# Kernel optimization log

Hardware: AMD Instinct MI355X
Metric: run time of the kernel (lower is better)

The kernel has to match this reference:

```python
import jax, jax.numpy as jnp
import numpy as np

LN_EPS = 1e-5  # torch nn.LayerNorm default


def setup_inputs() -> dict:
    key = jax.random.key(0)
    kx, kw = jax.random.split(key)
    tokens, d_in, d_out = 8192, 4096, 16384
    x = jax.random.normal(kx, (tokens, d_in), dtype=jnp.float32)
    # nn.Linear weight layout: [out_features, in_features]
    W = jax.random.normal(kw, (d_out, d_in), dtype=jnp.float32) * (1.0 / np.sqrt(d_in))
    return {"x": x, "W": W}


def reference(x, W):
    # LayerNorm over last dim, no affine params (elementwise_affine=False)
    mean = jnp.mean(x, axis=-1, keepdims=True)
    var = jnp.mean(jnp.square(x - mean), axis=-1, keepdims=True)  # biased, as torch LN
    xn = (x - mean) * jax.lax.rsqrt(var + LN_EPS)
    # Linear (no bias): [tokens, d_in] @ [d_in, d_out]
    y = jnp.einsum("td,od->to", xn, W)
    return jax.nn.sigmoid(y)
```

## Files before the change

kernel.cpp:

```cpp
#include <hip/hip_runtime.h>
#include <hip/hip_bf16.h>
#include <stdint.h>

#define TOKENS 8192
#define DIN    4096
#define DOUT   16384

#define BM 256
#define BN 256
#define BKT 64
#define NT (DIN / BKT)
#define NJ (NT / 2)

typedef short s16x8 __attribute__((ext_vector_type(8)));
typedef float f32x4 __attribute__((ext_vector_type(4)));

#define AS1 __attribute__((address_space(1)))
#define AS3 __attribute__((address_space(3)))
#define VMCNT(n)  asm volatile("s_waitcnt vmcnt(" #n ")" ::: "memory")
#define LGKM0()   asm volatile("s_waitcnt lgkmcnt(0)" ::: "memory")
#define SCHEDB()  __builtin_amdgcn_sched_barrier(0)
#define BAR()     __builtin_amdgcn_s_barrier()

__device__ __forceinline__ unsigned short f2bf(float f) {
  unsigned int u = __float_as_uint(f);
  u += 0x7fffu + ((u >> 16) & 1u);
  return (unsigned short)(u >> 16);
}

__global__ __launch_bounds__(256) void ln_kernel(const float* __restrict__ x,
                                                 unsigned short* __restrict__ xn) {
  const int row = blockIdx.x;
  const float4* xr = reinterpret_cast<const float4*>(x + (size_t)row * DIN);
  float4 v[4];
  float sum = 0.f, ssq = 0.f;
#pragma unroll
  for (int i = 0; i < 4; ++i) {
    v[i] = xr[threadIdx.x + i * 256];
    sum += v[i].x + v[i].y + v[i].z + v[i].w;
    ssq += v[i].x * v[i].x + v[i].y * v[i].y + v[i].z * v[i].z + v[i].w * v[i].w;
  }
#pragma unroll
  for (int off = 32; off > 0; off >>= 1) {
    sum += __shfl_xor(sum, off, 64);
    ssq += __shfl_xor(ssq, off, 64);
  }
  __shared__ float red[8];
  const int wid = threadIdx.x >> 6;
  if ((threadIdx.x & 63) == 0) { red[wid] = sum; red[wid + 4] = ssq; }
  __syncthreads();
  sum = red[0] + red[1] + red[2] + red[3];
  ssq = red[4] + red[5] + red[6] + red[7];
  const float mean = sum * (1.f / DIN);
  const float var  = ssq * (1.f / DIN) - mean * mean;
  const float rs   = rsqrtf(var + 1e-5f);
  ushort4* xo = reinterpret_cast<ushort4*>(xn + (size_t)row * DIN);
#pragma unroll
  for (int i = 0; i < 4; ++i) {
    ushort4 o;
    o.x = f2bf((v[i].x - mean) * rs);
    o.y = f2bf((v[i].y - mean) * rs);
    o.z = f2bf((v[i].z - mean) * rs);
    o.w = f2bf((v[i].w - mean) * rs);
    xo[threadIdx.x + i * 256] = o;
  }
}

__global__ __launch_bounds__(256) void cvt_kernel(const float* __restrict__ W,
                                                  unsigned short* __restrict__ Wb) {
  const size_t i = (size_t)blockIdx.x * 256 + threadIdx.x;
  float4 v = reinterpret_cast<const float4*>(W)[i];
  ushort4 o;
  o.x = f2bf(v.x); o.y = f2bf(v.y); o.z = f2bf(v.z); o.w = f2bf(v.w);
  reinterpret_cast<ushort4*>(Wb)[i] = o;
}

__global__ __launch_bounds__(512, 2) void gemm_sig(const unsigned short* __restrict__ A,
                                                   const unsigned short* __restrict__ B,
                                                   float* __restrict__ C) {
  __shared__ unsigned short Asl[2 * 256 * 64];
  __shared__ unsigned short Bsl[2 * 256 * 64];

  const int bid = blockIdx.x;
  const int cpx = gridDim.x >> 3;
  const int swz = (bid & 7) * cpx + (bid >> 3);
  const int bm = swz & 31;
  const int bn = swz >> 5;

  const int tid  = threadIdx.x;
  const int wid  = tid >> 6;
  const int lane = tid & 63;
  const int wr = wid >> 2, wc = wid & 3;

  const unsigned short* gA = A + (size_t)bm * BM * DIN;
  const unsigned short* gB = B + (size_t)bn * BN * DIN;

  const int l8 = lane >> 3, l7 = lane & 7;
  const int csw = l7 ^ l8;
  const unsigned short* sA0 = gA + (size_t)(wid * 8 + l8) * DIN + csw * 8;
  const unsigned short* sA1 = sA0 + (size_t)64 * DIN;
  const unsigned short* sB0 = gB + (size_t)(wid * 8 + l8) * DIN + csw * 8;
  const unsigned short* sB1 = sB0 + (size_t)64 * DIN;
  const int dOfs = wid * 512;

#define STG_A(p, h, kt) do { \
  __builtin_amdgcn_global_load_lds((const AS1 void*)(sA0 + (size_t)(h) * 128 * DIN + (kt) * BKT), \
      (AS3 void*)(Asl + ((p) * 256 + (h) * 128) * 64 + dOfs), 16, 0, 0); \
  __builtin_amdgcn_global_load_lds((const AS1 void*)(sA1 + (size_t)(h) * 128 * DIN + (kt) * BKT), \
      (AS3 void*)(Asl + ((p) * 256 + (h) * 128 + 64) * 64 + dOfs), 16, 0, 0); } while (0)
#define STG_B(p, h, kt) do { \
  __builtin_amdgcn_global_load_lds((const AS1 void*)(sB0 + (size_t)(h) * 128 * DIN + (kt) * BKT), \
      (AS3 void*)(Bsl + ((p) * 256 + (h) * 128) * 64 + dOfs), 16, 0, 0); \
  __builtin_amdgcn_global_load_lds((const AS1 void*)(sB1 + (size_t)(h) * 128 * DIN + (kt) * BKT), \
      (AS3 void*)(Bsl + ((p) * 256 + (h) * 128 + 64) * 64 + dOfs), 16, 0, 0); } while (0)

  const int aBase = (wr * 128 + (lane & 15)) * 64;
  const int bBase = (wc * 64 + (lane & 15)) * 64;
  const int slt0 = (((lane >> 4)) ^ l7) * 8;
  const int slt1 = (((lane >> 4) + 4) ^ l7) * 8;

  s16x8 af[4][2], bf[4][2];
  f32x4 acc[8][4] = {};

#define LDA(p, MB) do { _Pragma("unroll") for (int mm = 0; mm < 4; ++mm) { \
    const unsigned short* _b = Asl + (p) * 16384 + aBase + ((MB) + mm) * 1024; \
    af[mm][0] = *reinterpret_cast<const s16x8*>(_b + slt0); \
    af[mm][1] = *reinterpret_cast<const s16x8*>(_b + slt1); } } while (0)
#define LDB(p, NB) do { _Pragma("unroll") for (int nn = 0; nn < 2; ++nn) { \
    const unsigned short* _b = Bsl + (p) * 16384 + bBase + ((NB) + nn) * 1024; \
    bf[(NB) + nn][0] = *reinterpret_cast<const s16x8*>(_b + slt0); \
    bf[(NB) + nn][1] = *reinterpret_cast<const s16x8*>(_b + slt1); } } while (0)

#define QUAD(MB, NB) do { _Pragma("unroll") for (int mm = 0; mm < 4; ++mm) { \
    _Pragma("unroll") for (int nn = 0; nn < 2; ++nn) { \
      acc[(MB)+mm][(NB)+nn] = __builtin_amdgcn_mfma_f32_16x16x32_bf16(af[mm][0], bf[(NB)+nn][0], acc[(MB)+mm][(NB)+nn], 0, 0, 0); \
      acc[(MB)+mm][(NB)+nn] = __builtin_amdgcn_mfma_f32_16x16x32_bf16(af[mm][1], bf[(NB)+nn][1], acc[(MB)+mm][(NB)+nn], 0, 0, 0); } } } while (0)

#define PH_TOP()  SCHEDB(); BAR()
#define PH_BOT()  LGKM0(); SCHEDB(); BAR()

  STG_B(0, 0, 0); STG_B(0, 1, 0); STG_A(0, 0, 0); STG_A(0, 1, 0);
  STG_B(1, 0, 1); STG_B(1, 1, 1);
  VMCNT(4); SCHEDB(); BAR();

  for (int j = 0; j < NJ - 1; ++j) {
    const int t1 = 2 * j + 1, t2 = 2 * j + 2, t3 = 2 * j + 3;
    LDA(0, 0); LDB(0, 0); STG_A(1, 0, t1); PH_TOP();
    __builtin_amdgcn_s_setprio(1); QUAD(0, 0); __builtin_amdgcn_s_setprio(0); PH_BOT();
    LDB(0, 2); STG_A(1, 1, t1); PH_TOP();
    __builtin_amdgcn_s_setprio(1); QUAD(0, 2); __builtin_amdgcn_s_setprio(0); PH_BOT();
    LDA(0, 4); STG_B(0, 0, t2); PH_TOP();
    __builtin_amdgcn_s_setprio(1); QUAD(4, 0); __builtin_amdgcn_s_setprio(0); PH_BOT();
    STG_B(0, 1, t2); PH_TOP();
    __builtin_amdgcn_s_setprio(1); QUAD(4, 2); __builtin_amdgcn_s_setprio(0);
    LGKM0(); VMCNT(4); SCHEDB(); BAR();
    LDA(1, 0); LDB(1, 0); STG_A(0, 0, t2); PH_TOP();
    __builtin_amdgcn_s_setprio(1); QUAD(0, 0); __builtin_amdgcn_s_setprio(0); PH_BOT();
    LDB(1, 2); STG_A(0, 1, t2); PH_TOP();
    __builtin_amdgcn_s_setprio(1); QUAD(0, 2); __builtin_amdgcn_s_setprio(0); PH_BOT();
    LDA(1, 4); STG_B(1, 0, t3); PH_TOP();
    __builtin_amdgcn_s_setprio(1); QUAD(4, 0); __builtin_amdgcn_s_setprio(0); PH_BOT();
    STG_B(1, 1, t3); PH_TOP();
    __builtin_amdgcn_s_setprio(1); QUAD(4, 2); __builtin_amdgcn_s_setprio(0);
    LGKM0(); VMCNT(4); SCHEDB(); BAR();
  }

  {
    const int t1 = NT - 1;
    LDA(0, 0); LDB(0, 0); STG_A(1, 0, t1); PH_TOP();
    __builtin_amdgcn_s_setprio(1); QUAD(0, 0); __builtin_amdgcn_s_setprio(0); PH_BOT();
    LDB(0, 2); STG_A(1, 1, t1); PH_TOP();
    __builtin_amdgcn_s_setprio(1); QUAD(0, 2); __builtin_amdgcn_s_setprio(0); PH_BOT();
    LDA(0, 4); PH_TOP();
    __builtin_amdgcn_s_setprio(1); QUAD(4, 0); __builtin_amdgcn_s_setprio(0); PH_BOT();
    PH_TOP();
    __builtin_amdgcn_s_setprio(1); QUAD(4, 2); __builtin_amdgcn_s_setprio(0);
    LGKM0(); VMCNT(0); SCHEDB(); BAR();
    LDA(1, 0); LDB(1, 0); PH_TOP();
    __builtin_amdgcn_s_setprio(1); QUAD(0, 0); __builtin_amdgcn_s_setprio(0); PH_BOT();
    LDB(1, 2); PH_TOP();
    __builtin_amdgcn_s_setprio(1); QUAD(0, 2); __builtin_amdgcn_s_setprio(0); PH_BOT();
    LDA(1, 4); PH_TOP();
    __builtin_amdgcn_s_setprio(1); QUAD(4, 0); __builtin_amdgcn_s_setprio(0); PH_BOT();
    __builtin_amdgcn_s_setprio(1); QUAD(4, 2); __builtin_amdgcn_s_setprio(0);
  }

#undef STG_A
#undef STG_B
#undef LDA
#undef LDB
#undef QUAD
#undef PH_TOP
#undef PH_BOT

  const int crow0 = bm * BM + wr * 128 + (lane >> 4) * 4;
  const int ccol0 = bn * BN + wc * 64 + (lane & 15);
#pragma unroll
  for (int m = 0; m < 8; ++m)
#pragma unroll
    for (int n = 0; n < 4; ++n)
#pragma unroll
      for (int jj = 0; jj < 4; ++jj) {
        const float v = acc[m][n][jj];
        C[(size_t)(crow0 + m * 16 + jj) * DOUT + (ccol0 + n * 16)] = 1.f / (1.f + __expf(-v));
      }
}

extern "C" void kernel_launch(void* const* d_in, const int* in_sizes, int n_in,
                              void* d_out, int out_size, void* d_ws, size_t ws_size,
                              hipStream_t stream) {
  const float* x = (const float*)d_in[0];
  const float* W = (const float*)d_in[1];
  float* out = (float*)d_out;

  unsigned short* xn = (unsigned short*)d_ws;
  unsigned short* Wb = xn + (size_t)TOKENS * DIN;

  ln_kernel<<<TOKENS, 256, 0, stream>>>(x, xn);
  cvt_kernel<<<((size_t)DOUT * DIN) / 1024, 256, 0, stream>>>(W, Wb);
  gemm_sig<<<(TOKENS / BM) * (DOUT / BN), 512, 0, stream>>>(xn, Wb, out);
}
```

Baseline: 1.341 ms.

## Restructure GEMM main loop into k-half phases with finer-grained staged loads

Reorganizes the bf16 MFMA main loop so each phase reads one k-half of A and B fragments and issues 4x4 MFMA blocks, instead of 4x2 quads that each cover both k-halves. Global-to-LDS staging is split into quarter-tile loads spread across phases and guarded by vmcnt waits rather than lgkmcnt-zero barriers. The aim is better overlap of LDS reads, global loads and MFMA work with fewer register-held B fragments. It risks wrong vmcnt accounting, which could cause races or stalls, and it relies on the compiler inserting the LDS read waits that the removed lgkmcnt(0) used to provide.

```diff
diff --git a/kernel.cpp b/kernel.cpp
--- a/kernel.cpp
+++ b/kernel.cpp
@@ -18,7 +18,6 @@
 #define AS1 __attribute__((address_space(1)))
 #define AS3 __attribute__((address_space(3)))
 #define VMCNT(n)  asm volatile("s_waitcnt vmcnt(" #n ")" ::: "memory")
-#define LGKM0()   asm volatile("s_waitcnt lgkmcnt(0)" ::: "memory")
 #define SCHEDB()  __builtin_amdgcn_sched_barrier(0)
 #define BAR()     __builtin_amdgcn_s_barrier()
 
@@ -97,101 +96,96 @@
 
   const int l8 = lane >> 3, l7 = lane & 7;
   const int csw = l7 ^ l8;
-  const unsigned short* sA0 = gA + (size_t)(wid * 8 + l8) * DIN + csw * 8;
-  const unsigned short* sA1 = sA0 + (size_t)64 * DIN;
-  const unsigned short* sB0 = gB + (size_t)(wid * 8 + l8) * DIN + csw * 8;
-  const unsigned short* sB1 = sB0 + (size_t)64 * DIN;
+  const unsigned short* sA = gA + (size_t)(wid * 8 + l8) * DIN + csw * 8;
+  const unsigned short* sB = gB + (size_t)(wid * 8 + l8) * DIN + csw * 8;
   const int dOfs = wid * 512;
 
-#define STG_A(p, h, kt) do { \
-  __builtin_amdgcn_global_load_lds((const AS1 void*)(sA0 + (size_t)(h) * 128 * DIN + (kt) * BKT), \
-      (AS3 void*)(Asl + ((p) * 256 + (h) * 128) * 64 + dOfs), 16, 0, 0); \
-  __builtin_amdgcn_global_load_lds((const AS1 void*)(sA1 + (size_t)(h) * 128 * DIN + (kt) * BKT), \
-      (AS3 void*)(Asl + ((p) * 256 + (h) * 128 + 64) * 64 + dOfs), 16, 0, 0); } while (0)
-#define STG_B(p, h, kt) do { \
-  __builtin_amdgcn_global_load_lds((const AS1 void*)(sB0 + (size_t)(h) * 128 * DIN + (kt) * BKT), \
-      (AS3 void*)(Bsl + ((p) * 256 + (h) * 128) * 64 + dOfs), 16, 0, 0); \
-  __builtin_amdgcn_global_load_lds((const AS1 void*)(sB1 + (size_t)(h) * 128 * DIN + (kt) * BKT), \
-      (AS3 void*)(Bsl + ((p) * 256 + (h) * 128 + 64) * 64 + dOfs), 16, 0, 0); } while (0)
-
-  const int aBase = (wr * 128 + (lane & 15)) * 64;
-  const int bBase = (wc * 64 + (lane & 15)) * 64;
-  const int slt0 = (((lane >> 4)) ^ l7) * 8;
-  const int slt1 = (((lane >> 4) + 4) ^ l7) * 8;
-
-  s16x8 af[4][2], bf[4][2];
+#define STG_Aq(p, q, kt) __builtin_amdgcn_global_load_lds( \
+    (const AS1 void*)(sA + (size_t)(q) * 64 * DIN + (size_t)(kt) * BKT), \
+    (AS3 void*)(Asl + ((p) * 256 + (q) * 64) * 64 + dOfs), 16, 0, 0)
+#define STG_Bq(p, q, kt) __builtin_amdgcn_global_load_lds( \
+    (const AS1 void*)(sB + (size_t)(q) * 64 * DIN + (size_t)(kt) * BKT), \
+    (AS3 void*)(Bsl + ((p) * 256 + (q) * 64) * 64 + dOfs), 16, 0, 0)
+
+  int aO[8], bO[4], slt[2];
+#pragma unroll
+  for (int m = 0; m < 8; ++m) aO[m] = (wr * 128 + m * 16 + (lane & 15)) * 64;
+#pragma unroll
+  for (int n = 0; n < 4; ++n) bO[n] = (wc * 64 + n * 16 + (lane & 15)) * 64;
+  slt[0] = ((lane >> 4) ^ l7) * 8;
+  slt[1] = (((lane >> 4) + 4) ^ l7) * 8;
+
+  s16x8 af[4], bf0[4], bf1[4];
   f32x4 acc[8][4] = {};
 
-#define LDA(p, MB) do { _Pragma("unroll") for (int mm = 0; mm < 4; ++mm) { \
-    const unsigned short* _b = Asl + (p) * 16384 + aBase + ((MB) + mm) * 1024; \
-    af[mm][0] = *reinterpret_cast<const s16x8*>(_b + slt0); \
-    af[mm][1] = *reinterpret_cast<const s16x8*>(_b + slt1); } } while (0)
-#define LDB(p, NB) do { _Pragma("unroll") for (int nn = 0; nn < 2; ++nn) { \
-    const unsigned short* _b = Bsl + (p) * 16384 + bBase + ((NB) + nn) * 1024; \
-    bf[(NB) + nn][0] = *reinterpret_cast<const s16x8*>(_b + slt0); \
-    bf[(NB) + nn][1] = *reinterpret_cast<const s16x8*>(_b + slt1); } } while (0)
-
-#define QUAD(MB, NB) do { _Pragma("unroll") for (int mm = 0; mm < 4; ++mm) { \
-    _Pragma("unroll") for (int nn = 0; nn < 2; ++nn) { \
-      acc[(MB)+mm][(NB)+nn] = __builtin_amdgcn_mfma_f32_16x16x32_bf16(af[mm][0], bf[(NB)+nn][0], acc[(MB)+mm][(NB)+nn], 0, 0, 0); \
-      acc[(MB)+mm][(NB)+nn] = __builtin_amdgcn_mfma_f32_16x16x32_bf16(af[mm][1], bf[(NB)+nn][1], acc[(MB)+mm][(NB)+nn], 0, 0, 0); } } } while (0)
-
-#define PH_TOP()  SCHEDB(); BAR()
-#define PH_BOT()  LGKM0(); SCHEDB(); BAR()
-
-  STG_B(0, 0, 0); STG_B(0, 1, 0); STG_A(0, 0, 0); STG_A(0, 1, 0);
-  STG_B(1, 0, 1); STG_B(1, 1, 1);
-  VMCNT(4); SCHEDB(); BAR();
+#define RD_A(p, mb4, kh) do { _Pragma("unroll") for (int mm = 0; mm < 4; ++mm) \
+    af[mm] = *reinterpret_cast<const s16x8*>(Asl + (p) * 16384 + aO[(mb4) + mm] + slt[kh]); } while (0)
+#define RD_B(p, kh, dst) do { _Pragma("unroll") for (int nn = 0; nn < 4; ++nn) \
+    dst[nn] = *reinterpret_cast<const s16x8*>(Bsl + (p) * 16384 + bO[nn] + slt[kh]); } while (0)
+#define MM(mb4, bfr) do { _Pragma("unroll") for (int mm = 0; mm < 4; ++mm) \
+    _Pragma("unroll") for (int nn = 0; nn < 4; ++nn) \
+      acc[(mb4) + mm][nn] = __builtin_amdgcn_mfma_f32_16x16x32_bf16(af[mm], bfr[nn], acc[(mb4) + mm][nn], 0, 0, 0); } while (0)
+#define PRIO1() __builtin_amdgcn_s_setprio(1)
+#define PRIO0() __builtin_amdgcn_s_setprio(0)
+
+  STG_Aq(0, 0, 0); STG_Aq(0, 1, 0); STG_Aq(0, 2, 0); STG_Aq(0, 3, 0);
+  STG_Bq(0, 0, 0); STG_Bq(0, 1, 0); STG_Bq(0, 2, 0); STG_Bq(0, 3, 0);
+  STG_Aq(1, 0, 1); STG_Aq(1, 2, 1);
+  STG_Bq(1, 0, 1); STG_Bq(1, 1, 1); STG_Bq(1, 2, 1); STG_Bq(1, 3, 1);
+  VMCNT(6); SCHEDB(); BAR();
 
   for (int j = 0; j < NJ - 1; ++j) {
     const int t1 = 2 * j + 1, t2 = 2 * j + 2, t3 = 2 * j + 3;
-    LDA(0, 0); LDB(0, 0); STG_A(1, 0, t1); PH_TOP();
-    __builtin_amdgcn_s_setprio(1); QUAD(0, 0); __builtin_amdgcn_s_setprio(0); PH_BOT();
-    LDB(0, 2); STG_A(1, 1, t1); PH_TOP();
-    __builtin_amdgcn_s_setprio(1); QUAD(0, 2); __builtin_amdgcn_s_setprio(0); PH_BOT();
-    LDA(0, 4); STG_B(0, 0, t2); PH_TOP();
-    __builtin_amdgcn_s_setprio(1); QUAD(4, 0); __builtin_amdgcn_s_setprio(0); PH_BOT();
-    STG_B(0, 1, t2); PH_TOP();
-    __builtin_amdgcn_s_setprio(1); QUAD(4, 2); __builtin_amdgcn_s_setprio(0);
-    LGKM0(); VMCNT(4); SCHEDB(); BAR();
-    LDA(1, 0); LDB(1, 0); STG_A(0, 0, t2); PH_TOP();
-    __builtin_amdgcn_s_setprio(1); QUAD(0, 0); __builtin_amdgcn_s_setprio(0); PH_BOT();
-    LDB(1, 2); STG_A(0, 1, t2); PH_TOP();
-    __builtin_amdgcn_s_setprio(1); QUAD(0, 2); __builtin_amdgcn_s_setprio(0); PH_BOT();
-    LDA(1, 4); STG_B(1, 0, t3); PH_TOP();
-    __builtin_amdgcn_s_setprio(1); QUAD(4, 0); __builtin_amdgcn_s_setprio(0); PH_BOT();
-    STG_B(1, 1, t3); PH_TOP();
-    __builtin_amdgcn_s_setprio(1); QUAD(4, 2); __builtin_amdgcn_s_setprio(0);
-    LGKM0(); VMCNT(4); SCHEDB(); BAR();
+    VMCNT(8); RD_A(0, 0, 0); RD_B(0, 0, bf0);
+    STG_Aq(1, 1, t1); STG_Aq(1, 3, t1);
+    SCHEDB(); BAR(); PRIO1(); MM(0, bf0); PRIO0(); SCHEDB(); BAR();
+    VMCNT(8); RD_A(0, 0, 1); RD_B(0, 1, bf1);
+    SCHEDB(); BAR(); PRIO1(); MM(0, bf1); PRIO0(); SCHEDB(); BAR();
+    VMCNT(8); RD_A(0, 4, 0);
+    STG_Bq(0, 0, t2); STG_Bq(0, 1, t2); STG_Bq(0, 2, t2); STG_Bq(0, 3, t2);
+    STG_Aq(0, 0, t2); STG_Aq(0, 2, t2);
+    SCHEDB(); BAR(); PRIO1(); MM(4, bf0); PRIO0(); SCHEDB(); BAR();
+    VMCNT(8); RD_A(0, 4, 1);
+    SCHEDB(); BAR(); PRIO1(); MM(4, bf1); PRIO0(); SCHEDB(); BAR();
+    VMCNT(8); RD_A(1, 0, 0); RD_B(1, 0, bf0);
+    STG_Aq(0, 1, t2); STG_Aq(0, 3, t2);
+    SCHEDB(); BAR(); PRIO1(); MM(0, bf0); PRIO0(); SCHEDB(); BAR();
+    VMCNT(8); RD_A(1, 0, 1); RD_B(1, 1, bf1);
+    SCHEDB(); BAR(); PRIO1(); MM(0, bf1); PRIO0(); SCHEDB(); BAR();
+    VMCNT(8); RD_A(1, 4, 0);
+    STG_Bq(1, 0, t3); STG_Bq(1, 1, t3); STG_Bq(1, 2, t3); STG_Bq(1, 3, t3);
+    STG_Aq(1, 0, t3); STG_Aq(1, 2, t3);
+    SCHEDB(); BAR(); PRIO1(); MM(4, bf0); PRIO0(); SCHEDB(); BAR();
+    VMCNT(8); RD_A(1, 4, 1);
+    SCHEDB(); BAR(); PRIO1(); MM(4, bf1); PRIO0(); SCHEDB(); BAR();
   }
 
   {
     const int t1 = NT - 1;
-    LDA(0, 0); LDB(0, 0); STG_A(1, 0, t1); PH_TOP();
-    __builtin_amdgcn_s_setprio(1); QUAD(0, 0); __builtin_amdgcn_s_setprio(0); PH_BOT();
-    LDB(0, 2); STG_A(1, 1, t1); PH_TOP();
-    __builtin_amdgcn_s_setprio(1); QUAD(0, 2); __builtin_amdgcn_s_setprio(0); PH_BOT();
-    LDA(0, 4); PH_TOP();
-    __builtin_amdgcn_s_setprio(1); QUAD(4, 0); __builtin_amdgcn_s_setprio(0); PH_BOT();
-    PH_TOP();
-    __builtin_amdgcn_s_setprio(1); QUAD(4, 2); __builtin_amdgcn_s_setprio(0);
-    LGKM0(); VMCNT(0); SCHEDB(); BAR();
-    LDA(1, 0); LDB(1, 0); PH_TOP();
-    __builtin_amdgcn_s_setprio(1); QUAD(0, 0); __builtin_amdgcn_s_setprio(0); PH_BOT();
-    LDB(1, 2); PH_TOP();
-    __builtin_amdgcn_s_setprio(1); QUAD(0, 2); __builtin_amdgcn_s_setprio(0); PH_BOT();
-    LDA(1, 4); PH_TOP();
-    __builtin_amdgcn_s_setprio(1); QUAD(4, 0); __builtin_amdgcn_s_setprio(0); PH_BOT();
-    __builtin_amdgcn_s_setprio(1); QUAD(4, 2); __builtin_amdgcn_s_setprio(0);
-  }
-
-#undef STG_A
-#undef STG_B
-#undef LDA
-#undef LDB
-#undef QUAD
-#undef PH_TOP
-#undef PH_BOT
+    VMCNT(8); RD_A(0, 0, 0); RD_B(0, 0, bf0);
+    STG_Aq(1, 1, t1); STG_Aq(1, 3, t1);
+    SCHEDB(); BAR(); PRIO1(); MM(0, bf0); PRIO0(); SCHEDB(); BAR();
+    VMCNT(8); RD_A(0, 0, 1); RD_B(0, 1, bf1);
+    SCHEDB(); BAR(); PRIO1(); MM(0, bf1); PRIO0(); SCHEDB(); BAR();
+    VMCNT(8); RD_A(0, 4, 0);
+    SCHEDB(); BAR(); PRIO1(); MM(4, bf0); PRIO0(); SCHEDB(); BAR();
+    VMCNT(2); RD_A(0, 4, 1);
+    SCHEDB(); BAR(); PRIO1(); MM(4, bf1); PRIO0(); SCHEDB(); BAR();
+    VMCNT(2); RD_A(1, 0, 0); RD_B(1, 0, bf0);
+    SCHEDB(); BAR(); PRIO1(); MM(0, bf0); PRIO0(); SCHEDB(); BAR();
+    VMCNT(0); RD_A(1, 0, 1); RD_B(1, 1, bf1);
+    SCHEDB(); BAR(); PRIO1(); MM(0, bf1); PRIO0(); SCHEDB(); BAR();
+    VMCNT(0); RD_A(1, 4, 0);
+    SCHEDB(); BAR(); PRIO1(); MM(4, bf0); PRIO0(); SCHEDB(); BAR();
+    VMCNT(0); RD_A(1, 4, 1);
+    SCHEDB(); BAR(); PRIO1(); MM(4, bf1); PRIO0();
+  }
+
+#undef STG_Aq
+#undef STG_Bq
+#undef RD_A
+#undef RD_B
+#undef MM
 
   const int crow0 = bm * BM + wr * 128 + (lane >> 4) * 4;
   const int ccol0 = bn * BN + wc * 64 + (lane & 15);
```

New measurement: 1.351 ms. About the same (+0.7%).
